# Optimization experiments

Measured on AMD Instinct MI355X. Metric: run time of the kernel, lower is better.

## Reference

```python
import jax, jax.numpy as jnp
import numpy as np

N_HEADS = 16
EPSILON = 0.01
SCORE_SCALE = 1.0
C_CONST = 2.0 + EPSILON


def setup_inputs() -> dict:
    key = jax.random.key(0)
    k1, k2, k3 = jax.random.split(key, 3)
    B, T, D = 2, 2048, 1024
    x = jax.random.normal(k1, (B, T, D), dtype=jnp.float32)
    # torch nn.Linear convention: weight [out_features, in_features], y = x @ W.T
    Wqkv = jax.random.normal(k2, (3 * D, D), dtype=jnp.float32) * (1.0 / np.sqrt(D))
    Wout = jax.random.normal(k3, (D, D), dtype=jnp.float32) * (1.0 / np.sqrt(D))
    return {"x": x, "Wqkv": Wqkv, "Wout": Wout}


def reference(x, Wqkv, Wout):
    B, T, D = x.shape
    H = N_HEADS
    hd = D // H
    qkv = x @ Wqkv.T  # [B, T, 3D]
    q, k, v = jnp.split(qkv, 3, axis=-1)
    # [B, H, T, hd]
    q = q.reshape(B, T, H, hd).transpose(0, 2, 1, 3).astype(jnp.float32)
    k = k.reshape(B, T, H, hd).transpose(0, 2, 1, 3).astype(jnp.float32)
    v = v.reshape(B, T, H, hd).transpose(0, 2, 1, 3).astype(jnp.float32)
    # L2 normalize along head dim (F.normalize uses eps=1e-12 via clamp of norm)
    qn = q / jnp.maximum(jnp.linalg.norm(q, axis=-1, keepdims=True), 1e-12)
    kn = k / jnp.maximum(jnp.linalg.norm(k, axis=-1, keepdims=True), 1e-12)
    # full T x T kernel matrix per (batch, head)
    x_dot = jnp.einsum("bhtd,bhsd->bhts", qn, kn)
    denom = jnp.maximum(C_CONST - 2.0 * x_dot, 1e-6)
    K = (x_dot * x_dot) / denom * SCORE_SCALE
    causal = jnp.tril(jnp.ones((T, T), dtype=bool))  # keep lower triangle incl. diag
    K = jnp.where(causal[None, None, :, :], K, 0.0)
    numerator = jnp.einsum("bhts,bhsd->bhtd", K, v)
    denominator = jnp.sum(K, axis=-1, keepdims=True)
    out = numerator / (denominator + 1e-6)
    out = out.transpose(0, 2, 1, 3).reshape(B, T, D)
    return out @ Wout.T
```

## Files before the change

kernel.cpp:

```cpp
#include <hip/hip_runtime.h>
#include <hip/hip_bf16.h>

#define T_SEQ 2048
#define D_MODEL 1024
#define BT 4096
#define QKV_N 3072

typedef __attribute__((ext_vector_type(8))) short bf16x8;
typedef __attribute__((ext_vector_type(4))) short bf16x4;
typedef __attribute__((ext_vector_type(4))) float f32x4;

typedef unsigned int __attribute__((address_space(1))) as1_uint;
typedef unsigned int __attribute__((address_space(3))) as3_uint;

__device__ __forceinline__ unsigned short f2bf(float f) {
    unsigned u = __builtin_bit_cast(unsigned, f);
    u += 0x7fffu + ((u >> 16) & 1u);
    return (unsigned short)(u >> 16);
}
__device__ __forceinline__ float bf2f(unsigned short h) {
    unsigned u = ((unsigned)h) << 16;
    return __builtin_bit_cast(float, u);
}
__device__ __forceinline__ void gload_lds16(const void* g, void* l) {
    __builtin_amdgcn_global_load_lds((const as1_uint*)g, (as3_uint*)l, 16, 0, 0);
}
__device__ __forceinline__ unsigned cvtpk_bf16(float lo, float hi) {
    unsigned r;
    asm("v_cvt_pk_bf16_f32 %0, %1, %2" : "=v"(r) : "v"(lo), "v"(hi));
    return r;
}

__global__ __launch_bounds__(256) void cvt_bf16_3(const float* __restrict__ s0, unsigned short* __restrict__ d0, int n0,
                                                  const float* __restrict__ s1, unsigned short* __restrict__ d1, int n1,
                                                  const float* __restrict__ s2, unsigned short* __restrict__ d2, int n2) {
    int i = blockIdx.x * 256 + threadIdx.x;
    const float* s; unsigned short* d;
    if (i < n0) { s = s0; d = d0; }
    else if (i < n0 + n1) { i -= n0; s = s1; d = d1; }
    else if (i < n0 + n1 + n2) { i -= n0 + n1; s = s2; d = d2; }
    else return;
    const float4* sp = (const float4*)s + (size_t)i * 2;
    const float4 a = sp[0], b = sp[1];
    uint4 o;
    o.x = (unsigned)f2bf(a.x) | ((unsigned)f2bf(a.y) << 16);
    o.y = (unsigned)f2bf(a.z) | ((unsigned)f2bf(a.w) << 16);
    o.z = (unsigned)f2bf(b.x) | ((unsigned)f2bf(b.y) << 16);
    o.w = (unsigned)f2bf(b.z) | ((unsigned)f2bf(b.w) << 16);
    ((uint4*)d)[i] = o;
}

template<int OUT_BF16>
__global__ __launch_bounds__(256) void gemm_bt_mfma(const unsigned short* __restrict__ A,
                                                    const unsigned short* __restrict__ B,
                                                    void* __restrict__ Cout,
                                                    int M, int N, int K) {
    __shared__ unsigned short As[128 * 64];
    __shared__ unsigned short Bs[128 * 64];
    const int tid = threadIdx.x;
    const int w = tid >> 6;
    const int l = tid & 63;
    const int l15 = l & 15, l4 = l >> 4;

    const int nblocks = (M / 128) * (N / 128);
    const int cpx = nblocks >> 3;
    const int id2 = (blockIdx.x & 7) * cpx + (blockIdx.x >> 3);
    const int bm = (id2 & 31) * 128;
    const int bn = (id2 >> 5) * 128;

    const int wm = (w >> 1) * 64, wn = (w & 1) * 64;

    const f32x4 z = {0.f, 0.f, 0.f, 0.f};
    f32x4 acc[4][4];
#pragma unroll
    for (int m = 0; m < 4; ++m)
#pragma unroll
        for (int n = 0; n < 4; ++n) acc[m][n] = z;

    const int lrow = l >> 3;
    const int lslot = (l & 7) ^ (lrow & 7);

    for (int k0 = 0; k0 < K; k0 += 64) {
#pragma unroll
        for (int i = 0; i < 4; ++i) {
            const int row = w * 32 + i * 8 + lrow;
            gload_lds16(A + (size_t)(bm + row) * K + k0 + lslot * 8, As + (w * 4 + i) * 512);
            gload_lds16(B + (size_t)(bn + row) * K + k0 + lslot * 8, Bs + (w * 4 + i) * 512);
        }
        __syncthreads();
        bf16x8 af[4][2], bfr[4][2];
#pragma unroll
        for (int m = 0; m < 4; ++m) {
            const int row = wm + m * 16 + l15;
            af[m][0] = *(const bf16x8*)(As + row * 64 + ((l4 ^ (row & 7)) * 8));
            af[m][1] = *(const bf16x8*)(As + row * 64 + (((4 + l4) ^ (row & 7)) * 8));
        }
#pragma unroll
        for (int n = 0; n < 4; ++n) {
            const int row = wn + n * 16 + l15;
            bfr[n][0] = *(const bf16x8*)(Bs + row * 64 + ((l4 ^ (row & 7)) * 8));
            bfr[n][1] = *(const bf16x8*)(Bs + row * 64 + (((4 + l4) ^ (row & 7)) * 8));
        }
#pragma unroll
        for (int m = 0; m < 4; ++m)
#pragma unroll
            for (int n = 0; n < 4; ++n) {
                acc[m][n] = __builtin_amdgcn_mfma_f32_16x16x32_bf16(af[m][0], bfr[n][0], acc[m][n], 0, 0, 0);
                acc[m][n] = __builtin_amdgcn_mfma_f32_16x16x32_bf16(af[m][1], bfr[n][1], acc[m][n], 0, 0, 0);
            }
        __syncthreads();
    }
#pragma unroll
    for (int m = 0; m < 4; ++m)
#pragma unroll
        for (int n = 0; n < 4; ++n)
#pragma unroll
            for (int r = 0; r < 4; ++r) {
                const int row = bm + wm + m * 16 + l4 * 4 + r;
                const int col = bn + wn + n * 16 + l15;
                if (OUT_BF16)
                    ((unsigned short*)Cout)[(size_t)row * N + col] = f2bf(acc[m][n][r]);
                else
                    ((float*)Cout)[(size_t)row * N + col] = acc[m][n][r];
            }
}

__global__ __launch_bounds__(256) void l2norm_qk_cvt(const unsigned short* __restrict__ qkvb,
                                                     unsigned short* __restrict__ qb,
                                                     unsigned short* __restrict__ kb) {
    const int wid = blockIdx.x * 4 + (threadIdx.x >> 6);
    const int lane = threadIdx.x & 63;
    const int sel = wid & 1;
    const int h = (wid >> 1) & 15;
    const int n = wid >> 5;
    const float v = bf2f(qkvb[(size_t)n * QKV_N + sel * D_MODEL + h * 64 + lane]);
    float ss = v * v;
#pragma unroll
    for (int off = 32; off; off >>= 1) ss += __shfl_xor(ss, off);
    const float sc = 1.0f / fmaxf(sqrtf(ss), 1e-12f);
    const int b = n >> 11, t = n & 2047;
    unsigned short* dst = (sel ? kb : qb) + (((size_t)(b * 16 + h) * T_SEQ + t) * 64) + lane;
    *dst = f2bf(v * sc);
}

__global__ __launch_bounds__(256) void v_cvt_T(const unsigned short* __restrict__ qkvb,
                                               unsigned short* __restrict__ vbT) {
    __shared__ unsigned short tile[64][72];
    const int bh = blockIdx.y;
    const int b = bh >> 4, h = bh & 15;
    const int t0 = blockIdx.x * 64;
    const int r = threadIdx.x >> 2;
    const int c = (threadIdx.x & 3) * 16;
    const unsigned short* src = qkvb + (size_t)(b * T_SEQ + t0 + r) * QKV_N + 2 * D_MODEL + h * 64 + c;
    uint4 v0 = *(const uint4*)(src);
    uint4 v1 = *(const uint4*)(src + 8);
    unsigned short tmp[16];
    *(uint4*)tmp = v0;
    *(uint4*)(tmp + 8) = v1;
#pragma unroll
    for (int j = 0; j < 16; ++j) tile[c + j][r] = tmp[j];
    __syncthreads();
    const int d = threadIdx.x >> 2;
    const int tc = (threadIdx.x & 3) * 16;
    unsigned short tmp2[16];
#pragma unroll
    for (int j = 0; j < 16; ++j) tmp2[j] = tile[d][tc + j];
    unsigned short* dst = vbT + ((size_t)bh * 64 + d) * T_SEQ + t0 + tc;
    *(uint4*)dst = *(uint4*)tmp2;
    *(uint4*)(dst + 8) = *(uint4*)(tmp2 + 8);
}

#define AT_TS 64

__global__ __launch_bounds__(256) void attn_mfma(const unsigned short* __restrict__ qb,
                                                 const unsigned short* __restrict__ kb,
                                                 const unsigned short* __restrict__ vbT,
                                                 unsigned short* __restrict__ attnb) {
    __shared__ unsigned short Ks[2][64 * 64];
    __shared__ unsigned short Vs[2][64 * 64];

    const int tid = threadIdx.x;
    const int w = tid >> 6;
    const int l = tid & 63;
    const int l15 = l & 15, l4 = l >> 4;

    const int id = blockIdx.x;
    const int xcd = id & 7;
    const int within = id >> 3;
    const int bh = xcd * 4 + (within & 3);
    const int t0i = 31 - (within >> 2);
    const int t0 = t0i * 64;

    const size_t hb = (size_t)bh * T_SEQ * 64;
    const unsigned short* kb_h = kb + hb;
    const unsigned short* vb_h = vbT + hb;

    const int lrow = l >> 3;
    const int lslot = (l & 7) ^ (lrow & 7);

    bf16x8 qf0, qf1;
    {
        const unsigned short* qp = qb + hb + (size_t)(t0 + w * 16 + l15) * 64 + l4 * 8;
        qf0 = *(const bf16x8*)(qp);
        qf1 = *(const bf16x8*)(qp + 32);
    }

    const f32x4 z = {0.f, 0.f, 0.f, 0.f};
    f32x4 acc[4];
#pragma unroll
    for (int i = 0; i < 4; ++i) acc[i] = z;
    float accd = 0.f;

    const int wrow0 = t0 + w * 16;
    const int tq = wrow0 + l15;
    const int nst = t0i + 1;

#pragma unroll
    for (int c = 0; c < 2; ++c) {
        const int row = w * 16 + c * 8 + lrow;
        gload_lds16(kb_h + (size_t)row * 64 + lslot * 8, &Ks[0][(w * 2 + c) * 512]);
        gload_lds16(vb_h + (size_t)row * T_SEQ + lslot * 8, &Vs[0][(w * 2 + c) * 512]);
    }

    for (int st = 0; st < nst; ++st) {
        const int cur = st & 1;
        const int s0 = st * AT_TS;
        if (st + 1 < nst) {
            const int sn = (st + 1) * AT_TS;
#pragma unroll
            for (int c = 0; c < 2; ++c) {
                const int row = w * 16 + c * 8 + lrow;
                gload_lds16(kb_h + (size_t)(sn + row) * 64 + lslot * 8, &Ks[cur ^ 1][(w * 2 + c) * 512]);
                gload_lds16(vb_h + (size_t)row * T_SEQ + sn + lslot * 8, &Vs[cur ^ 1][(w * 2 + c) * 512]);
            }
            asm volatile("s_waitcnt vmcnt(4)" ::: "memory");
        } else {
            asm volatile("s_waitcnt vmcnt(0)" ::: "memory");
        }
        __builtin_amdgcn_sched_barrier(0);
        __builtin_amdgcn_s_barrier();

        const unsigned short* Kc = &Ks[cur][0];
        f32x4 sC[4];
#pragma unroll
        for (int sf = 0; sf < 4; ++sf) {
            const int row = sf * 16 + l15;
            bf16x8 kf0 = *(const bf16x8*)(Kc + row * 64 + ((l4 ^ (row & 7)) * 8));
            bf16x8 kf1 = *(const bf16x8*)(Kc + row * 64 + (((4 + l4) ^ (row & 7)) * 8));
            f32x4 c = z;
            c = __builtin_amdgcn_mfma_f32_16x16x32_bf16(kf0, qf0, c, 0, 0, 0);
            c = __builtin_amdgcn_mfma_f32_16x16x32_bf16(kf1, qf1, c, 0, 0, 0);
            sC[sf] = c;
        }

        const bool need_mask = (s0 + AT_TS - 1 > wrow0);
        float part = 0.f;
#pragma unroll
        for (int sf = 0; sf < 4; ++sf)
#pragma unroll
            for (int r = 0; r < 4; ++r) {
                const float xd = sC[sf][r];
                const float den = __builtin_fmaf(-2.0f, xd, 2.01f);
                float Kv = xd * xd * __builtin_amdgcn_rcpf(den);
                if (need_mask) {
                    const int s = s0 + sf * 16 + l4 * 4 + r;
                    if (s > tq) Kv = 0.f;
                }
                part += Kv;
                sC[sf][r] = Kv;
            }
        accd += part;

        uint4 p0, p1;
        p0.x = cvtpk_bf16(sC[0][0], sC[0][1]);
        p0.y = cvtpk_bf16(sC[0][2], sC[0][3]);
        p0.z = cvtpk_bf16(sC[1][0], sC[1][1]);
        p0.w = cvtpk_bf16(sC[1][2], sC[1][3]);
        p1.x = cvtpk_bf16(sC[2][0], sC[2][1]);
        p1.y = cvtpk_bf16(sC[2][2], sC[2][3]);
        p1.z = cvtpk_bf16(sC[3][0], sC[3][1]);
        p1.w = cvtpk_bf16(sC[3][2], sC[3][3]);
        const bf16x8 a0 = __builtin_bit_cast(bf16x8, p0);
        const bf16x8 a1 = __builtin_bit_cast(bf16x8, p1);

        const unsigned short* Vc = &Vs[cur][0];
#pragma unroll
        for (int df = 0; df < 4; ++df) {
            const int row = df * 16 + l15;
            const int p = row & 7;
            const int base = row * 64;
            const int off = (l4 & 1) * 4;
            bf16x4 v0 = *(const bf16x4*)(Vc + base + (((l4 >> 1) + 0) ^ p) * 8 + off);
            bf16x4 v1 = *(const bf16x4*)(Vc + base + (((l4 >> 1) + 2) ^ p) * 8 + off);
            bf16x4 v2 = *(const bf16x4*)(Vc + base + (((l4 >> 1) + 4) ^ p) * 8 + off);
            bf16x4 v3 = *(const bf16x4*)(Vc + base + (((l4 >> 1) + 6) ^ p) * 8 + off);
            bf16x8 B0, B1;
#pragma unroll
            for (int j = 0; j < 4; ++j) {
                B0[j] = v0[j]; B0[j + 4] = v1[j];
                B1[j] = v2[j]; B1[j + 4] = v3[j];
            }
            acc[df] = __builtin_amdgcn_mfma_f32_16x16x32_bf16(a0, B0, acc[df], 0, 0, 0);
            acc[df] = __builtin_amdgcn_mfma_f32_16x16x32_bf16(a1, B1, acc[df], 0, 0, 0);
        }
        __builtin_amdgcn_sched_barrier(0);
        __builtin_amdgcn_s_barrier();
    }

    accd += __shfl_xor(accd, 16);
    accd += __shfl_xor(accd, 32);

    const int b = bh >> 4, h = bh & 15;
#pragma unroll
    for (int r = 0; r < 4; ++r) {
        const float den = __shfl(accd, l4 * 4 + r) + 1e-6f;
#pragma unroll
        for (int df = 0; df < 4; ++df) {
            const int t = wrow0 + l4 * 4 + r;
            const float o = acc[df][r] / den;
            attnb[((size_t)b * T_SEQ + t) * D_MODEL + h * 64 + df * 16 + l15] = f2bf(o);
        }
    }
}

extern "C" void kernel_launch(void* const* d_in, const int* in_sizes, int n_in,
                              void* d_out, int out_size, void* d_ws, size_t ws_size,
                              hipStream_t stream) {
    const float* x    = (const float*)d_in[0];
    const float* Wqkv = (const float*)d_in[1];
    const float* Wout = (const float*)d_in[2];
    float* out = (float*)d_out;

    char* ws = (char*)d_ws;
    unsigned short* xb    = (unsigned short*)(ws);
    unsigned short* wqkvb = (unsigned short*)(ws + (size_t)8 * 1024 * 1024);
    unsigned short* qkvb  = (unsigned short*)(ws + (size_t)16 * 1024 * 1024);
    unsigned short* vbT   = (unsigned short*)(ws + (size_t)40 * 1024 * 1024);
    unsigned short* woutb = (unsigned short*)(ws + (size_t)48 * 1024 * 1024);
    unsigned short* qbp   = xb;
    unsigned short* kbp   = wqkvb;
    unsigned short* attnb = qkvb;

    cvt_bf16_3<<<4096, 256, 0, stream>>>(x, xb, BT * D_MODEL / 8,
                                         Wqkv, wqkvb, QKV_N * D_MODEL / 8,
                                         Wout, woutb, D_MODEL * D_MODEL / 8);

    gemm_bt_mfma<1><<<(QKV_N / 128) * (BT / 128), 256, 0, stream>>>(xb, wqkvb, qkvb, BT, QKV_N, D_MODEL);

    l2norm_qk_cvt<<<BT * 32 / 4, 256, 0, stream>>>(qkvb, qbp, kbp);
    v_cvt_T<<<dim3(T_SEQ / 64, 32), 256, 0, stream>>>(qkvb, vbT);

    attn_mfma<<<1024, 256, 0, stream>>>(qbp, kbp, vbT, attnb);

    gemm_bt_mfma<0><<<(D_MODEL / 128) * (BT / 128), 256, 0, stream>>>(attnb, woutb, out, BT, D_MODEL, D_MODEL);
}
```

Before: 205.6 us.

## Fuse Q/K L2-normalization into QKV GEMM epilogue and restructure attention loop

```diff
diff --git a/kernel.cpp b/kernel.cpp
--- a/kernel.cpp
+++ b/kernel.cpp
@@ -50,10 +50,12 @@
     ((uint4*)d)[i] = o;
 }
 
-template<int OUT_BF16>
+template<int MODE>
 __global__ __launch_bounds__(256) void gemm_bt_mfma(const unsigned short* __restrict__ A,
                                                     const unsigned short* __restrict__ B,
                                                     void* __restrict__ Cout,
+                                                    unsigned short* __restrict__ qbp,
+                                                    unsigned short* __restrict__ kbp,
                                                     int M, int N, int K) {
     __shared__ unsigned short As[128 * 64];
     __shared__ unsigned short Bs[128 * 64];
@@ -110,40 +112,59 @@
             }
         __syncthreads();
     }
-#pragma unroll
-    for (int m = 0; m < 4; ++m)
-#pragma unroll
-        for (int n = 0; n < 4; ++n)
-#pragma unroll
-            for (int r = 0; r < 4; ++r) {
-                const int row = bm + wm + m * 16 + l4 * 4 + r;
-                const int col = bn + wn + n * 16 + l15;
-                if (OUT_BF16)
-                    ((unsigned short*)Cout)[(size_t)row * N + col] = f2bf(acc[m][n][r]);
-                else
+
+    if (MODE == 0) {
+#pragma unroll
+        for (int m = 0; m < 4; ++m)
+#pragma unroll
+            for (int n = 0; n < 4; ++n)
+#pragma unroll
+                for (int r = 0; r < 4; ++r) {
+                    const int row = bm + wm + m * 16 + l4 * 4 + r;
+                    const int col = bn + wn + n * 16 + l15;
                     ((float*)Cout)[(size_t)row * N + col] = acc[m][n][r];
-            }
-}
-
-__global__ __launch_bounds__(256) void l2norm_qk_cvt(const unsigned short* __restrict__ qkvb,
-                                                     unsigned short* __restrict__ qb,
-                                                     unsigned short* __restrict__ kb) {
-    const int wid = blockIdx.x * 4 + (threadIdx.x >> 6);
-    const int lane = threadIdx.x & 63;
-    const int sel = wid & 1;
-    const int h = (wid >> 1) & 15;
-    const int n = wid >> 5;
-    const float v = bf2f(qkvb[(size_t)n * QKV_N + sel * D_MODEL + h * 64 + lane]);
-    float ss = v * v;
-#pragma unroll
-    for (int off = 32; off; off >>= 1) ss += __shfl_xor(ss, off);
-    const float sc = 1.0f / fmaxf(sqrtf(ss), 1e-12f);
-    const int b = n >> 11, t = n & 2047;
-    unsigned short* dst = (sel ? kb : qb) + (((size_t)(b * 16 + h) * T_SEQ + t) * 64) + lane;
-    *dst = f2bf(v * sc);
-}
-
-__global__ __launch_bounds__(256) void v_cvt_T(const unsigned short* __restrict__ qkvb,
+                }
+    } else {
+        const int gcol0 = bn + wn;
+        const int part = gcol0 >> 10;
+        const int h = (gcol0 >> 6) & 15;
+        if (part < 2) {
+            unsigned short* dst = part ? kbp : qbp;
+#pragma unroll
+            for (int m = 0; m < 4; ++m)
+#pragma unroll
+                for (int r = 0; r < 4; ++r) {
+                    float ss = 0.f;
+#pragma unroll
+                    for (int n = 0; n < 4; ++n) ss = fmaf(acc[m][n][r], acc[m][n][r], ss);
+                    ss += __shfl_xor(ss, 1);
+                    ss += __shfl_xor(ss, 2);
+                    ss += __shfl_xor(ss, 4);
+                    ss += __shfl_xor(ss, 8);
+                    const float sc = 1.0f / fmaxf(sqrtf(ss), 1e-12f);
+                    const int row = bm + wm + m * 16 + l4 * 4 + r;
+                    const int bh2 = (row >> 11) * 16 + h;
+                    unsigned short* pdst = dst + ((size_t)bh2 * T_SEQ + (row & 2047)) * 64 + l15;
+#pragma unroll
+                    for (int n = 0; n < 4; ++n) pdst[n * 16] = f2bf(acc[m][n][r] * sc);
+                }
+        } else {
+            unsigned short* vrow = (unsigned short*)Cout;
+            const int vcol0 = gcol0 - 2048;
+#pragma unroll
+            for (int m = 0; m < 4; ++m)
+#pragma unroll
+                for (int n = 0; n < 4; ++n)
+#pragma unroll
+                    for (int r = 0; r < 4; ++r) {
+                        const int row = bm + wm + m * 16 + l4 * 4 + r;
+                        vrow[(size_t)row * D_MODEL + vcol0 + n * 16 + l15] = f2bf(acc[m][n][r]);
+                    }
+        }
+    }
+}
+
+__global__ __launch_bounds__(256) void v_cvt_T(const unsigned short* __restrict__ vrow,
                                                unsigned short* __restrict__ vbT) {
     __shared__ unsigned short tile[64][72];
     const int bh = blockIdx.y;
@@ -151,7 +172,7 @@
     const int t0 = blockIdx.x * 64;
     const int r = threadIdx.x >> 2;
     const int c = (threadIdx.x & 3) * 16;
-    const unsigned short* src = qkvb + (size_t)(b * T_SEQ + t0 + r) * QKV_N + 2 * D_MODEL + h * 64 + c;
+    const unsigned short* src = vrow + (size_t)(b * T_SEQ + t0 + r) * D_MODEL + h * 64 + c;
     uint4 v0 = *(const uint4*)(src);
     uint4 v1 = *(const uint4*)(src + 8);
     unsigned short tmp[16];
@@ -192,11 +213,29 @@
     const int t0 = t0i * 64;
 
     const size_t hb = (size_t)bh * T_SEQ * 64;
-    const unsigned short* kb_h = kb + hb;
-    const unsigned short* vb_h = vbT + hb;
 
     const int lrow = l >> 3;
     const int lslot = (l & 7) ^ (lrow & 7);
+    const unsigned short* kgp[2];
+    const unsigned short* vgp[2];
+    unsigned short* kdst[2];
+    unsigned short* vdst[2];
+#pragma unroll
+    for (int c = 0; c < 2; ++c) {
+        const int row = w * 16 + c * 8 + lrow;
+        kgp[c] = kb + hb + (size_t)row * 64 + lslot * 8;
+        vgp[c] = vbT + hb + (size_t)row * T_SEQ + lslot * 8;
+        kdst[c] = &Ks[0][(w * 2 + c) * 512];
+        vdst[c] = &Vs[0][(w * 2 + c) * 512];
+    }
+
+    const int p = l15 & 7;
+    const unsigned short* kfp0 = &Ks[0][0] + l15 * 64 + ((l4 ^ p) * 8);
+    const unsigned short* kfp1 = &Ks[0][0] + l15 * 64 + (((4 + l4) ^ p) * 8);
+    const unsigned short* vfp0 = &Vs[0][0] + l15 * 64 + ((((l4 >> 1) + 0) ^ p) * 8) + (l4 & 1) * 4;
+    const unsigned short* vfp1 = &Vs[0][0] + l15 * 64 + ((((l4 >> 1) + 2) ^ p) * 8) + (l4 & 1) * 4;
+    const unsigned short* vfp2 = &Vs[0][0] + l15 * 64 + ((((l4 >> 1) + 4) ^ p) * 8) + (l4 & 1) * 4;
+    const unsigned short* vfp3 = &Vs[0][0] + l15 * 64 + ((((l4 >> 1) + 6) ^ p) * 8) + (l4 & 1) * 4;
 
     bf16x8 qf0, qf1;
     {
@@ -213,48 +252,27 @@
 
     const int wrow0 = t0 + w * 16;
     const int tq = wrow0 + l15;
-    const int nst = t0i + 1;
 
 #pragma unroll
     for (int c = 0; c < 2; ++c) {
-        const int row = w * 16 + c * 8 + lrow;
-        gload_lds16(kb_h + (size_t)row * 64 + lslot * 8, &Ks[0][(w * 2 + c) * 512]);
-        gload_lds16(vb_h + (size_t)row * T_SEQ + lslot * 8, &Vs[0][(w * 2 + c) * 512]);
-    }
-
-    for (int st = 0; st < nst; ++st) {
-        const int cur = st & 1;
-        const int s0 = st * AT_TS;
-        if (st + 1 < nst) {
-            const int sn = (st + 1) * AT_TS;
-#pragma unroll
-            for (int c = 0; c < 2; ++c) {
-                const int row = w * 16 + c * 8 + lrow;
-                gload_lds16(kb_h + (size_t)(sn + row) * 64 + lslot * 8, &Ks[cur ^ 1][(w * 2 + c) * 512]);
-                gload_lds16(vb_h + (size_t)row * T_SEQ + sn + lslot * 8, &Vs[cur ^ 1][(w * 2 + c) * 512]);
-            }
-            asm volatile("s_waitcnt vmcnt(4)" ::: "memory");
-        } else {
-            asm volatile("s_waitcnt vmcnt(0)" ::: "memory");
-        }
-        __builtin_amdgcn_sched_barrier(0);
-        __builtin_amdgcn_s_barrier();
-
-        const unsigned short* Kc = &Ks[cur][0];
+        gload_lds16(kgp[c], kdst[c]);
+        gload_lds16(vgp[c], vdst[c]);
+    }
+
+    auto compute_tile = [&](int roff, int s0, bool mask) {
+        const unsigned short* kc0 = kfp0 + roff;
+        const unsigned short* kc1 = kfp1 + roff;
         f32x4 sC[4];
 #pragma unroll
         for (int sf = 0; sf < 4; ++sf) {
-            const int row = sf * 16 + l15;
-            bf16x8 kf0 = *(const bf16x8*)(Kc + row * 64 + ((l4 ^ (row & 7)) * 8));
-            bf16x8 kf1 = *(const bf16x8*)(Kc + row * 64 + (((4 + l4) ^ (row & 7)) * 8));
+            bf16x8 kf0 = *(const bf16x8*)(kc0 + sf * 1024);
+            bf16x8 kf1 = *(const bf16x8*)(kc1 + sf * 1024);
             f32x4 c = z;
             c = __builtin_amdgcn_mfma_f32_16x16x32_bf16(kf0, qf0, c, 0, 0, 0);
             c = __builtin_amdgcn_mfma_f32_16x16x32_bf16(kf1, qf1, c, 0, 0, 0);
             sC[sf] = c;
         }
-
-        const bool need_mask = (s0 + AT_TS - 1 > wrow0);
-        float part = 0.f;
+        float part_ = 0.f;
 #pragma unroll
         for (int sf = 0; sf < 4; ++sf)
 #pragma unroll
@@ -262,15 +280,14 @@
                 const float xd = sC[sf][r];
                 const float den = __builtin_fmaf(-2.0f, xd, 2.01f);
                 float Kv = xd * xd * __builtin_amdgcn_rcpf(den);
-                if (need_mask) {
+                if (mask) {
                     const int s = s0 + sf * 16 + l4 * 4 + r;
                     if (s > tq) Kv = 0.f;
                 }
-                part += Kv;
+                part_ += Kv;
                 sC[sf][r] = Kv;
             }
-        accd += part;
-
+        accd += part_;
         uint4 p0, p1;
         p0.x = cvtpk_bf16(sC[0][0], sC[0][1]);
         p0.y = cvtpk_bf16(sC[0][2], sC[0][3]);
@@ -282,29 +299,47 @@
         p1.w = cvtpk_bf16(sC[3][2], sC[3][3]);
         const bf16x8 a0 = __builtin_bit_cast(bf16x8, p0);
         const bf16x8 a1 = __builtin_bit_cast(bf16x8, p1);
-
-        const unsigned short* Vc = &Vs[cur][0];
+        const unsigned short* vc0 = vfp0 + roff;
+        const unsigned short* vc1 = vfp1 + roff;
+        const unsigned short* vc2 = vfp2 + roff;
+        const unsigned short* vc3 = vfp3 + roff;
 #pragma unroll
         for (int df = 0; df < 4; ++df) {
-            const int row = df * 16 + l15;
-            const int p = row & 7;
-            const int base = row * 64;
-            const int off = (l4 & 1) * 4;
-            bf16x4 v0 = *(const bf16x4*)(Vc + base + (((l4 >> 1) + 0) ^ p) * 8 + off);
-            bf16x4 v1 = *(const bf16x4*)(Vc + base + (((l4 >> 1) + 2) ^ p) * 8 + off);
-            bf16x4 v2 = *(const bf16x4*)(Vc + base + (((l4 >> 1) + 4) ^ p) * 8 + off);
-            bf16x4 v3 = *(const bf16x4*)(Vc + base + (((l4 >> 1) + 6) ^ p) * 8 + off);
-            bf16x8 B0, B1;
-#pragma unroll
-            for (int j = 0; j < 4; ++j) {
-                B0[j] = v0[j]; B0[j + 4] = v1[j];
-                B1[j] = v2[j]; B1[j + 4] = v3[j];
-            }
+            const uint2 u0 = *(const uint2*)(vc0 + df * 1024);
+            const uint2 u1 = *(const uint2*)(vc1 + df * 1024);
+            const uint2 u2 = *(const uint2*)(vc2 + df * 1024);
+            const uint2 u3 = *(const uint2*)(vc3 + df * 1024);
+            uint4 b0v, b1v;
+            b0v.x = u0.x; b0v.y = u0.y; b0v.z = u1.x; b0v.w = u1.y;
+            b1v.x = u2.x; b1v.y = u2.y; b1v.z = u3.x; b1v.w = u3.y;
+            const bf16x8 B0 = __builtin_bit_cast(bf16x8, b0v);
+            const bf16x8 B1 = __builtin_bit_cast(bf16x8, b1v);
             acc[df] = __builtin_amdgcn_mfma_f32_16x16x32_bf16(a0, B0, acc[df], 0, 0, 0);
             acc[df] = __builtin_amdgcn_mfma_f32_16x16x32_bf16(a1, B1, acc[df], 0, 0, 0);
         }
+    };
+
+    for (int st = 0; st < t0i; ++st) {
+        const int dsto = ((st & 1) ^ 1) * 4096;
+#pragma unroll
+        for (int c = 0; c < 2; ++c) {
+            kgp[c] += 4096;
+            vgp[c] += 64;
+            gload_lds16(kgp[c], kdst[c] + dsto);
+            gload_lds16(vgp[c], vdst[c] + dsto);
+        }
+        asm volatile("s_waitcnt vmcnt(4)" ::: "memory");
         __builtin_amdgcn_sched_barrier(0);
         __builtin_amdgcn_s_barrier();
+        compute_tile((st & 1) * 4096, st * AT_TS, false);
+        __builtin_amdgcn_sched_barrier(0);
+        __builtin_amdgcn_s_barrier();
+    }
+    {
+        asm volatile("s_waitcnt vmcnt(0)" ::: "memory");
+        __builtin_amdgcn_sched_barrier(0);
+        __builtin_amdgcn_s_barrier();
+        compute_tile((t0i & 1) * 4096, t0i * AT_TS, true);
     }
 
     accd += __shfl_xor(accd, 16);
@@ -334,23 +369,24 @@
     char* ws = (char*)d_ws;
     unsigned short* xb    = (unsigned short*)(ws);
     unsigned short* wqkvb = (unsigned short*)(ws + (size_t)8 * 1024 * 1024);
-    unsigned short* qkvb  = (unsigned short*)(ws + (size_t)16 * 1024 * 1024);
-    unsigned short* vbT   = (unsigned short*)(ws + (size_t)40 * 1024 * 1024);
-    unsigned short* woutb = (unsigned short*)(ws + (size_t)48 * 1024 * 1024);
-    unsigned short* qbp   = xb;
-    unsigned short* kbp   = wqkvb;
-    unsigned short* attnb = qkvb;
+    unsigned short* vrow  = (unsigned short*)(ws + (size_t)16 * 1024 * 1024);
+    unsigned short* vbT   = (unsigned short*)(ws + (size_t)24 * 1024 * 1024);
+    unsigned short* woutb = (unsigned short*)(ws + (size_t)32 * 1024 * 1024);
+    unsigned short* qbp   = (unsigned short*)(ws + (size_t)34 * 1024 * 1024);
+    unsigned short* kbp   = (unsigned short*)(ws + (size_t)42 * 1024 * 1024);
+    unsigned short* attnb = (unsigned short*)(ws + (size_t)50 * 1024 * 1024);
 
     cvt_bf16_3<<<4096, 256, 0, stream>>>(x, xb, BT * D_MODEL / 8,
                                          Wqkv, wqkvb, QKV_N * D_MODEL / 8,
                                          Wout, woutb, D_MODEL * D_MODEL / 8);
 
-    gemm_bt_mfma<1><<<(QKV_N / 128) * (BT / 128), 256, 0, stream>>>(xb, wqkvb, qkvb, BT, QKV_N, D_MODEL);
-
-    l2norm_qk_cvt<<<BT * 32 / 4, 256, 0, stream>>>(qkvb, qbp, kbp);
-    v_cvt_T<<<dim3(T_SEQ / 64, 32), 256, 0, stream>>>(qkvb, vbT);
+    gemm_bt_mfma<2><<<(QKV_N / 128) * (BT / 128), 256, 0, stream>>>(
+        xb, wqkvb, vrow, qbp, kbp, BT, QKV_N, D_MODEL);
+
+    v_cvt_T<<<dim3(T_SEQ / 64, 32), 256, 0, stream>>>(vrow, vbT);
 
     attn_mfma<<<1024, 256, 0, stream>>>(qbp, kbp, vbT, attnb);
 
-    gemm_bt_mfma<0><<<(D_MODEL / 128) * (BT / 128), 256, 0, stream>>>(attnb, woutb, out, BT, D_MODEL, D_MODEL);
-}
+    gemm_bt_mfma<0><<<(D_MODEL / 128) * (BT / 128), 256, 0, stream>>>(
+        attnb, woutb, out, nullptr, nullptr, BT, D_MODEL, D_MODEL);
+}
```

New measurement: 179.9 us. -12.5%, faster.
